# Performance work log

Measured on AMD Instinct MI355X. Metric: run time of the kernel, lower is better.

Reference implementation:

```python
import jax, jax.numpy as jnp
import numpy as np

ALPHA = 0.2   # LeakyReLU negative slope
NEG = -1e9    # mask value for non-edges


def setup_inputs() -> dict:
    key = jax.random.key(0)
    ks = jax.random.split(key, 8)
    N, Din, F, H, Dout = 4096, 512, 64, 8, 16
    adj = (jax.random.uniform(ks[0], (N, N)) < 0.01).astype(jnp.float32)
    adjacency = jnp.maximum(adj, jnp.eye(N, dtype=jnp.float32))
    X = jax.random.normal(ks[1], (N, Din), jnp.float32)
    s = lambda k, shape, fan: jax.random.normal(k, shape, jnp.float32) / np.float32(np.sqrt(fan))
    W = s(ks[2], (H, Din, F), Din)        # per-head projection, stacked
    a1 = s(ks[3], (H, F), F)              # attention vector, source half
    a2 = s(ks[4], (H, F), F)              # attention vector, target half
    Wo = s(ks[5], (H * F, Dout), H * F)   # output-layer projection
    ao1 = s(ks[6], (Dout,), Dout)
    ao2 = s(ks[7], (Dout,), Dout)
    return dict(adjacency=adjacency, X=X, W=W, a1=a1, a2=a2, Wo=Wo, ao1=ao1, ao2=ao2)


def reference(adjacency, X, W, a1, a2, Wo, ao1, ao2):
    # dropout is identity (eval mode / p=0)
    mask = adjacency > 0
    N = X.shape[0]
    # --- multi-head attention layers (concat=True -> ELU) ---
    Wh = jnp.einsum('nd,hdf->hnf', X, W)                      # [H, N, F]
    f1 = jnp.einsum('hnf,hf->hn', Wh, a1)                     # [H, N]
    f2 = jnp.einsum('hnf,hf->hn', Wh, a2)                     # [H, N]
    e = jax.nn.leaky_relu(f1[:, :, None] + f2[:, None, :], ALPHA)  # [H, N, N]
    att = jax.nn.softmax(jnp.where(mask[None], e, NEG), axis=-1)
    heads = jax.nn.elu(jnp.einsum('hnm,hmf->hnf', att, Wh))   # [H, N, F]
    cat = jnp.transpose(heads, (1, 0, 2)).reshape(N, -1)      # [N, H*F]
    # --- output attention layer (concat=False -> no ELU) ---
    Who = cat @ Wo                                            # [N, Dout]
    eo = jax.nn.leaky_relu((Who @ ao1)[:, None] + (Who @ ao2)[None, :], ALPHA)
    atto = jax.nn.softmax(jnp.where(mask, eo, NEG), axis=-1)  # [N, N]
    return atto @ Who                                         # [N, Dout]
```

## Files before the change

kernel.cpp:

```cpp
#include <hip/hip_runtime.h>
#include <hip/hip_bf16.h>

#define N_NODES 4096
#define DIN     512
#define FDIM    64
#define NHEADS  8
#define DOUT    16
#define MAXN    512

typedef __attribute__((ext_vector_type(8))) short bf16x8;
typedef __attribute__((ext_vector_type(4))) float f32x4;

static __device__ __forceinline__ float us2f(unsigned short u) {
    union { unsigned int i; float f; } cv; cv.i = ((unsigned int)u) << 16; return cv.f;
}
static __device__ __forceinline__ unsigned short f2us(float v) {
    __hip_bfloat16 b = __float2bfloat16(v);
    return *(const unsigned short*)&b;
}

__global__ __launch_bounds__(256) void setup_kernel(
    const void* __restrict__ adjv,
    const void* __restrict__ a1, const void* __restrict__ a2, const void* __restrict__ Wo,
    const void* __restrict__ ao1, const void* __restrict__ ao2,
    int* __restrict__ flag, float* __restrict__ dst,
    unsigned short* __restrict__ WtH, unsigned short* __restrict__ WtL)
{
    __shared__ int sflag;
    if (threadIdx.x == 0) {
        int f = (((const unsigned short*)adjv)[0] == 0) ? 1 : 0;
        *flag = f;
        sflag = f;
    }
    __syncthreads();
    const int f32 = sflag;
    const void* srcs[5] = { a1, a2, Wo, ao1, ao2 };
    const int   szs[5]  = { 512, 512, 8192, 16, 16 };
    int base = 0;
    for (int s = 0; s < 5; ++s) {
        if (f32) {
            for (int i = threadIdx.x; i < szs[s]; i += 256)
                dst[base + i] = ((const float*)srcs[s])[i];
        } else {
            for (int i = threadIdx.x; i < szs[s]; i += 256)
                dst[base + i] = us2f(((const unsigned short*)srcs[s])[i]);
        }
        base += szs[s];
    }
    __syncthreads();
    const float* Woc = dst + 1024;
    for (int l = threadIdx.x; l < DIN * DOUT; l += 256) {
        int d = l >> 4, j = l & 15;
        float v = Woc[l];
        unsigned short hi = f2us(v);
        WtH[j * DIN + d] = hi;
        WtL[j * DIN + d] = f2us(v - us2f(hi));
    }
}

__global__ __launch_bounds__(256) void build_nbr_kernel(
    const void* __restrict__ adj, const int* __restrict__ flag,
    int* __restrict__ cnt, int* __restrict__ nbr)
{
    const int n = blockIdx.x;
    const int f32 = *flag;
    __shared__ int c;
    if (threadIdx.x == 0) c = 0;
    __syncthreads();
    if (f32) {
        const uint4* row = (const uint4*)((const unsigned int*)adj + (size_t)n * N_NODES);
        for (int q = threadIdx.x; q < N_NODES / 4; q += 256) {
            uint4 v = row[q];
            int base = q * 4;
            if (v.x) { int p = atomicAdd(&c, 1); if (p < MAXN) nbr[(size_t)n * MAXN + p] = base + 0; }
            if (v.y) { int p = atomicAdd(&c, 1); if (p < MAXN) nbr[(size_t)n * MAXN + p] = base + 1; }
            if (v.z) { int p = atomicAdd(&c, 1); if (p < MAXN) nbr[(size_t)n * MAXN + p] = base + 2; }
            if (v.w) { int p = atomicAdd(&c, 1); if (p < MAXN) nbr[(size_t)n * MAXN + p] = base + 3; }
        }
    } else {
        const ushort4* row = (const ushort4*)((const unsigned short*)adj + (size_t)n * N_NODES);
        for (int q = threadIdx.x; q < N_NODES / 4; q += 256) {
            ushort4 v = row[q];
            int base = q * 4;
            if (v.x) { int p = atomicAdd(&c, 1); if (p < MAXN) nbr[(size_t)n * MAXN + p] = base + 0; }
            if (v.y) { int p = atomicAdd(&c, 1); if (p < MAXN) nbr[(size_t)n * MAXN + p] = base + 1; }
            if (v.z) { int p = atomicAdd(&c, 1); if (p < MAXN) nbr[(size_t)n * MAXN + p] = base + 2; }
            if (v.w) { int p = atomicAdd(&c, 1); if (p < MAXN) nbr[(size_t)n * MAXN + p] = base + 3; }
        }
    }
    __syncthreads();
    if (threadIdx.x == 0) cnt[n] = (c < MAXN) ? c : MAXN;
}

__global__ __launch_bounds__(256) void wh_mfma_kernel(
    const void* __restrict__ X, const void* __restrict__ W,
    const int* __restrict__ flag, unsigned short* __restrict__ Whb)
{
    __shared__ unsigned short Ah[64][72];
    __shared__ unsigned short Al[64][72];
    __shared__ unsigned short Bt[64][72];
    const int f32 = *flag;
    const int h  = blockIdx.x;
    const int bm = blockIdx.y;
    const int tid  = threadIdx.x;
    const int w    = tid >> 6;
    const int lane = tid & 63;
    const int quad = lane >> 4;
    const int l16  = lane & 15;
    const int r  = tid >> 2;
    const int c4 = (tid & 3) * 16;

    f32x4 acc[4];
#pragma unroll
    for (int j = 0; j < 4; ++j) acc[j] = (f32x4){0.f, 0.f, 0.f, 0.f};

    for (int k0 = 0; k0 < DIN; k0 += 64) {
        if (f32) {
            const float* xp = (const float*)X + (size_t)(bm * 64 + r) * DIN + k0 + c4;
            const float* wp = (const float*)W + (size_t)h * DIN * FDIM + (size_t)(k0 + r) * FDIM + c4;
#pragma unroll
            for (int i4 = 0; i4 < 4; ++i4) {
                float4 v4 = ((const float4*)xp)[i4];
                float vv[4] = { v4.x, v4.y, v4.z, v4.w };
#pragma unroll
                for (int t = 0; t < 4; ++t) {
                    int i = i4 * 4 + t;
                    unsigned short hi = f2us(vv[t]);
                    Ah[r][c4 + i] = hi;
                    Al[r][c4 + i] = f2us(vv[t] - us2f(hi));
                }
            }
#pragma unroll
            for (int i4 = 0; i4 < 4; ++i4) {
                float4 v4 = ((const float4*)wp)[i4];
                Bt[c4 + i4 * 4 + 0][r] = f2us(v4.x);
                Bt[c4 + i4 * 4 + 1][r] = f2us(v4.y);
                Bt[c4 + i4 * 4 + 2][r] = f2us(v4.z);
                Bt[c4 + i4 * 4 + 3][r] = f2us(v4.w);
            }
        } else {
            const unsigned short* xp = (const unsigned short*)X + (size_t)(bm * 64 + r) * DIN + k0 + c4;
            const unsigned short* wp = (const unsigned short*)W + (size_t)h * DIN * FDIM + (size_t)(k0 + r) * FDIM + c4;
#pragma unroll
            for (int i = 0; i < 16; ++i) { Ah[r][c4 + i] = xp[i]; Al[r][c4 + i] = 0; }
#pragma unroll
            for (int i = 0; i < 16; ++i) Bt[c4 + i][r] = wp[i];
        }
        __syncthreads();
#pragma unroll
        for (int kk = 0; kk < 64; kk += 32) {
            bf16x8 a_hi = *(const bf16x8*)&Ah[w * 16 + l16][kk + quad * 8];
            bf16x8 a_lo = *(const bf16x8*)&Al[w * 16 + l16][kk + quad * 8];
#pragma unroll
            for (int j = 0; j < 4; ++j) {
                bf16x8 b = *(const bf16x8*)&Bt[j * 16 + l16][kk + quad * 8];
                acc[j] = __builtin_amdgcn_mfma_f32_16x16x32_bf16(a_hi, b, acc[j], 0, 0, 0);
                acc[j] = __builtin_amdgcn_mfma_f32_16x16x32_bf16(a_lo, b, acc[j], 0, 0, 0);
            }
        }
        __syncthreads();
    }
#pragma unroll
    for (int j = 0; j < 4; ++j) {
        int col = j * 16 + l16;
#pragma unroll
        for (int rr = 0; rr < 4; ++rr) {
            int row = bm * 64 + w * 16 + quad * 4 + rr;
            Whb[((size_t)h * N_NODES + row) * FDIM + col] = f2us(acc[j][rr]);
        }
    }
}

__global__ __launch_bounds__(128) void f12_kernel(
    const unsigned short* __restrict__ Whb,
    const float* __restrict__ a1c, const float* __restrict__ a2c,
    float* __restrict__ f1, float* __restrict__ f2)
{
    int idx = blockIdx.x * 128 + threadIdx.x;
    int h = idx >> 12;
    const bf16x8* row = (const bf16x8*)(Whb + (size_t)idx * FDIM);
    float s1 = 0.f, s2 = 0.f;
#pragma unroll
    for (int q = 0; q < 8; ++q) {
        bf16x8 v8 = row[q];
#pragma unroll
        for (int t = 0; t < 8; ++t) {
            float v = us2f((unsigned short)v8[t]);
            int f = q * 8 + t;
            s1 += v * a1c[h * FDIM + f];
            s2 += v * a2c[h * FDIM + f];
        }
    }
    f1[idx] = s1;
    f2[idx] = s2;
}

__global__ __launch_bounds__(256) void attn1_kernel(
    const unsigned short* __restrict__ Whb,
    const float* __restrict__ f1, const float* __restrict__ f2,
    const int* __restrict__ cnt, const int* __restrict__ nbr,
    unsigned short* __restrict__ catb)
{
    const int n = blockIdx.x;
    const int tid = threadIdx.x;
    const int wid = tid >> 6;
    const int lane = tid & 63;
    __shared__ int sh_m[MAXN];
    __shared__ float sh_s[4][MAXN];
    const int c0 = cnt[n];
    const int c = (c0 < MAXN) ? c0 : MAXN;
    for (int k = tid; k < c; k += 256) sh_m[k] = nbr[(size_t)n * MAXN + k];
    __syncthreads();
    for (int hh = 0; hh < 2; ++hh) {
        const int h = wid * 2 + hh;
        const float f1v = f1[h * N_NODES + n];
        float mx = -1e30f;
        for (int k = lane; k < c; k += 64) {
            float s = f1v + f2[h * N_NODES + sh_m[k]];
            s = (s >= 0.f) ? s : 0.2f * s;
            sh_s[wid][k] = s;
            mx = fmaxf(mx, s);
        }
#pragma unroll
        for (int off = 32; off; off >>= 1) mx = fmaxf(mx, __shfl_xor(mx, off));
        float sum = 0.f;
        for (int k = lane; k < c; k += 64) {
            float e = __expf(sh_s[wid][k] - mx);
            sh_s[wid][k] = e;
            sum += e;
        }
#pragma unroll
        for (int off = 32; off; off >>= 1) sum += __shfl_xor(sum, off);
        const float inv = (sum > 0.f) ? 1.f / sum : 0.f;
        float acc = 0.f;
        for (int k = 0; k < c; ++k)
            acc += sh_s[wid][k] * us2f(Whb[((size_t)h * N_NODES + sh_m[k]) * FDIM + lane]);
        acc *= inv;
        acc = (acc > 0.f) ? acc : expm1f(acc);
        catb[(size_t)n * (NHEADS * FDIM) + h * FDIM + lane] = f2us(acc);
        __syncthreads();
    }
}

__global__ __launch_bounds__(64) void who_mfma_g_kernel(
    const unsigned short* __restrict__ catb,
    const unsigned short* __restrict__ WtH, const unsigned short* __restrict__ WtL,
    const float* __restrict__ ao1c, const float* __restrict__ ao2c,
    float* __restrict__ Who, float* __restrict__ g1, float* __restrict__ g2)
{
    const int lane = threadIdx.x;
    const int quad = lane >> 4, l16 = lane & 15;
    const int row0 = blockIdx.x * 16;
    f32x4 acc = (f32x4){0.f, 0.f, 0.f, 0.f};
    for (int k0 = 0; k0 < DIN; k0 += 32) {
        bf16x8 a  = *(const bf16x8*)&catb[(size_t)(row0 + l16) * DIN + k0 + quad * 8];
        bf16x8 bh = *(const bf16x8*)&WtH[l16 * DIN + k0 + quad * 8];
        bf16x8 bl = *(const bf16x8*)&WtL[l16 * DIN + k0 + quad * 8];
        acc = __builtin_amdgcn_mfma_f32_16x16x32_bf16(a, bh, acc, 0, 0, 0);
        acc = __builtin_amdgcn_mfma_f32_16x16x32_bf16(a, bl, acc, 0, 0, 0);
    }
#pragma unroll
    for (int rr = 0; rr < 4; ++rr) {
        int row = row0 + quad * 4 + rr;
        float v = acc[rr];
        Who[row * DOUT + l16] = v;
        float p1 = v * ao1c[l16];
        float p2 = v * ao2c[l16];
#pragma unroll
        for (int off = 8; off; off >>= 1) {
            p1 += __shfl_xor(p1, off);
            p2 += __shfl_xor(p2, off);
        }
        if (l16 == 0) { g1[row] = p1; g2[row] = p2; }
    }
}

__global__ __launch_bounds__(64) void attn2_kernel(
    const float* __restrict__ Who,
    const float* __restrict__ g1, const float* __restrict__ g2,
    const int* __restrict__ cnt, const int* __restrict__ nbr,
    const int* __restrict__ flag, void* __restrict__ out)
{
    const int n = blockIdx.x;
    const int lane = threadIdx.x;
    const int quad = lane >> 4, l16 = lane & 15;
    __shared__ float sh_s[MAXN];
    __shared__ int sh_m[MAXN];
    const int c0 = cnt[n];
    const int c = (c0 < MAXN) ? c0 : MAXN;
    for (int k = lane; k < c; k += 64) sh_m[k] = nbr[(size_t)n * MAXN + k];
    __syncthreads();
    const float gn = g1[n];
    float mx = -1e30f;
    for (int k = lane; k < c; k += 64) {
        float s = gn + g2[sh_m[k]];
        s = (s >= 0.f) ? s : 0.2f * s;
        sh_s[k] = s;
        mx = fmaxf(mx, s);
    }
#pragma unroll
    for (int off = 32; off; off >>= 1) mx = fmaxf(mx, __shfl_xor(mx, off));
    __syncthreads();
    float sum = 0.f;
    for (int k = lane; k < c; k += 64) {
        float e = __expf(sh_s[k] - mx);
        sh_s[k] = e;
        sum += e;
    }
#pragma unroll
    for (int off = 32; off; off >>= 1) sum += __shfl_xor(sum, off);
    __syncthreads();
    const float inv = (sum > 0.f) ? 1.f / sum : 0.f;
    float accv = 0.f;
    for (int k = quad; k < c; k += 4)
        accv += sh_s[k] * Who[sh_m[k] * DOUT + l16];
    accv += __shfl_xor(accv, 16);
    accv += __shfl_xor(accv, 32);
    if (quad == 0) {
        float v = accv * inv;
        if (*flag) ((float*)out)[n * DOUT + l16] = v;
        else       ((unsigned short*)out)[n * DOUT + l16] = f2us(v);
    }
}

__global__ void wsfail_kernel(float* __restrict__ out)
{
    if (threadIdx.x == 0) out[0] = 129.f;
}

extern "C" void kernel_launch(void* const* d_in, const int* in_sizes, int n_in,
                              void* d_out, int out_size, void* d_ws, size_t ws_size,
                              hipStream_t stream)
{
    const void* adj = d_in[0];
    const void* X   = d_in[1];
    const void* W   = d_in[2];
    const void* a1  = d_in[3];
    const void* a2  = d_in[4];
    const void* Wo  = d_in[5];
    const void* ao1 = d_in[6];
    const void* ao2 = d_in[7];

    const size_t NEEDED = 17500000;
    if (ws_size < NEEDED) { wsfail_kernel<<<1, 64, 0, stream>>>((float*)d_out); return; }

    int* flag = (int*)d_ws;
    int* cnt  = flag + 1;
    int* nbr  = cnt + 4096;
    float* smalls = (float*)(nbr + 2097152);
    float* a1c  = smalls;
    float* a2c  = smalls + 512;
    float* ao1c = smalls + 9216;
    float* ao2c = smalls + 9232;
    float* f1   = smalls + 9248;
    float* f2   = f1 + 32768;
    float* Who  = f2 + 32768;
    float* g1   = Who + 65536;
    float* g2   = g1 + 4096;
    unsigned short* Whb  = (unsigned short*)(g2 + 4096);
    unsigned short* catb = Whb + 2097152;
    unsigned short* WtH  = catb + 2097152;
    unsigned short* WtL  = WtH + 8192;

    setup_kernel<<<1, 256, 0, stream>>>(adj, a1, a2, Wo, ao1, ao2, flag, smalls, WtH, WtL);
    build_nbr_kernel<<<N_NODES, 256, 0, stream>>>(adj, flag, cnt, nbr);
    wh_mfma_kernel<<<dim3(NHEADS, N_NODES / 64), 256, 0, stream>>>(X, W, flag, Whb);
    f12_kernel<<<256, 128, 0, stream>>>(Whb, a1c, a2c, f1, f2);
    attn1_kernel<<<N_NODES, 256, 0, stream>>>(Whb, f1, f2, cnt, nbr, catb);
    who_mfma_g_kernel<<<N_NODES / 16, 64, 0, stream>>>(catb, WtH, WtL, ao1c, ao2c, Who, g1, g2);
    attn2_kernel<<<N_NODES, 64, 0, stream>>>(Who, g1, g2, cnt, nbr, flag, d_out);
}
```

Measured before the change: 183.7 us.

## Pre-split inputs in a wide prep kernel, node-major Wh, all-heads attn1

Replaces the single-block setup kernel with a grid-wide prep kernel that converts X into bf16 hi/lo halves and writes W transposed, so the Wh MFMA kernel reads operands directly from global memory without LDS staging or barriers. Wh is stored node-major ([N, H, F]), so attn1 processes all eight heads per block and each neighbor gather becomes one contiguous 1 KB row read instead of eight strided ones. The flag buffer is dropped in favor of detecting dtype from the adjacency in every kernel. This adds about 9 MB of workspace traffic for the pre-split X and skips LDS reuse of A/B tiles in the GEMM.

```diff
diff --git a/kernel.cpp b/kernel.cpp
--- a/kernel.cpp
+++ b/kernel.cpp
@@ -18,52 +18,56 @@
     __hip_bfloat16 b = __float2bfloat16(v);
     return *(const unsigned short*)&b;
 }
-
-__global__ __launch_bounds__(256) void setup_kernel(
-    const void* __restrict__ adjv,
+static __device__ __forceinline__ int is_f32(const void* adj) {
+    return (((const unsigned short*)adj)[0] == 0) ? 1 : 0;
+}
+
+__global__ __launch_bounds__(256) void prep_kernel(
+    const void* __restrict__ adj, const void* __restrict__ X, const void* __restrict__ W,
     const void* __restrict__ a1, const void* __restrict__ a2, const void* __restrict__ Wo,
     const void* __restrict__ ao1, const void* __restrict__ ao2,
-    int* __restrict__ flag, float* __restrict__ dst,
-    unsigned short* __restrict__ WtH, unsigned short* __restrict__ WtL)
-{
-    __shared__ int sflag;
-    if (threadIdx.x == 0) {
-        int f = (((const unsigned short*)adjv)[0] == 0) ? 1 : 0;
-        *flag = f;
-        sflag = f;
-    }
-    __syncthreads();
-    const int f32 = sflag;
-    const void* srcs[5] = { a1, a2, Wo, ao1, ao2 };
-    const int   szs[5]  = { 512, 512, 8192, 16, 16 };
-    int base = 0;
-    for (int s = 0; s < 5; ++s) {
-        if (f32) {
-            for (int i = threadIdx.x; i < szs[s]; i += 256)
-                dst[base + i] = ((const float*)srcs[s])[i];
-        } else {
-            for (int i = threadIdx.x; i < szs[s]; i += 256)
-                dst[base + i] = us2f(((const unsigned short*)srcs[s])[i]);
-        }
-        base += szs[s];
-    }
-    __syncthreads();
-    const float* Woc = dst + 1024;
-    for (int l = threadIdx.x; l < DIN * DOUT; l += 256) {
-        int d = l >> 4, j = l & 15;
-        float v = Woc[l];
+    unsigned short* __restrict__ Xhi, unsigned short* __restrict__ Xlo,
+    unsigned short* __restrict__ Wt,
+    unsigned short* __restrict__ WtH, unsigned short* __restrict__ WtL,
+    float* __restrict__ a1c, float* __restrict__ a2c,
+    float* __restrict__ ao1c, float* __restrict__ ao2c)
+{
+    const int f32 = is_f32(adj);
+    const int i0 = blockIdx.x * 256 + threadIdx.x;
+    const int T = gridDim.x * 256;
+    for (int i = i0; i < N_NODES * DIN; i += T) {
+        float v = f32 ? ((const float*)X)[i] : us2f(((const unsigned short*)X)[i]);
+        unsigned short hi = f2us(v);
+        Xhi[i] = hi;
+        Xlo[i] = f2us(v - us2f(hi));
+    }
+    for (int i = i0; i < NHEADS * DIN * FDIM; i += T) {
+        int hh = i >> 15, rem = i & 32767, d = rem >> 6, f = rem & 63;
+        float v = f32 ? ((const float*)W)[i] : us2f(((const unsigned short*)W)[i]);
+        Wt[((size_t)(hh * FDIM + f)) * DIN + d] = f2us(v);
+    }
+    for (int i = i0; i < DIN * DOUT; i += T) {
+        int d = i >> 4, j = i & 15;
+        float v = f32 ? ((const float*)Wo)[i] : us2f(((const unsigned short*)Wo)[i]);
         unsigned short hi = f2us(v);
         WtH[j * DIN + d] = hi;
         WtL[j * DIN + d] = f2us(v - us2f(hi));
     }
+    if (i0 < 512) {
+        a1c[i0] = f32 ? ((const float*)a1)[i0] : us2f(((const unsigned short*)a1)[i0]);
+        a2c[i0] = f32 ? ((const float*)a2)[i0] : us2f(((const unsigned short*)a2)[i0]);
+    }
+    if (i0 < 16) {
+        ao1c[i0] = f32 ? ((const float*)ao1)[i0] : us2f(((const unsigned short*)ao1)[i0]);
+        ao2c[i0] = f32 ? ((const float*)ao2)[i0] : us2f(((const unsigned short*)ao2)[i0]);
+    }
 }
 
 __global__ __launch_bounds__(256) void build_nbr_kernel(
-    const void* __restrict__ adj, const int* __restrict__ flag,
-    int* __restrict__ cnt, int* __restrict__ nbr)
+    const void* __restrict__ adj, int* __restrict__ cnt, int* __restrict__ nbr)
 {
     const int n = blockIdx.x;
-    const int f32 = *flag;
+    const int f32 = is_f32(adj);
     __shared__ int c;
     if (threadIdx.x == 0) c = 0;
     __syncthreads();
@@ -93,72 +97,34 @@
 }
 
 __global__ __launch_bounds__(256) void wh_mfma_kernel(
-    const void* __restrict__ X, const void* __restrict__ W,
-    const int* __restrict__ flag, unsigned short* __restrict__ Whb)
-{
-    __shared__ unsigned short Ah[64][72];
-    __shared__ unsigned short Al[64][72];
-    __shared__ unsigned short Bt[64][72];
-    const int f32 = *flag;
+    const unsigned short* __restrict__ Xhi, const unsigned short* __restrict__ Xlo,
+    const unsigned short* __restrict__ Wt, unsigned short* __restrict__ Whb)
+{
     const int h  = blockIdx.x;
     const int bm = blockIdx.y;
-    const int tid  = threadIdx.x;
-    const int w    = tid >> 6;
-    const int lane = tid & 63;
+    const int w    = threadIdx.x >> 6;
+    const int lane = threadIdx.x & 63;
     const int quad = lane >> 4;
     const int l16  = lane & 15;
-    const int r  = tid >> 2;
-    const int c4 = (tid & 3) * 16;
+    const int rowA = bm * 64 + w * 16 + l16;
 
     f32x4 acc[4];
 #pragma unroll
     for (int j = 0; j < 4; ++j) acc[j] = (f32x4){0.f, 0.f, 0.f, 0.f};
 
-    for (int k0 = 0; k0 < DIN; k0 += 64) {
-        if (f32) {
-            const float* xp = (const float*)X + (size_t)(bm * 64 + r) * DIN + k0 + c4;
-            const float* wp = (const float*)W + (size_t)h * DIN * FDIM + (size_t)(k0 + r) * FDIM + c4;
-#pragma unroll
-            for (int i4 = 0; i4 < 4; ++i4) {
-                float4 v4 = ((const float4*)xp)[i4];
-                float vv[4] = { v4.x, v4.y, v4.z, v4.w };
-#pragma unroll
-                for (int t = 0; t < 4; ++t) {
-                    int i = i4 * 4 + t;
-                    unsigned short hi = f2us(vv[t]);
-                    Ah[r][c4 + i] = hi;
-                    Al[r][c4 + i] = f2us(vv[t] - us2f(hi));
-                }
-            }
-#pragma unroll
-            for (int i4 = 0; i4 < 4; ++i4) {
-                float4 v4 = ((const float4*)wp)[i4];
-                Bt[c4 + i4 * 4 + 0][r] = f2us(v4.x);
-                Bt[c4 + i4 * 4 + 1][r] = f2us(v4.y);
-                Bt[c4 + i4 * 4 + 2][r] = f2us(v4.z);
-                Bt[c4 + i4 * 4 + 3][r] = f2us(v4.w);
-            }
-        } else {
-            const unsigned short* xp = (const unsigned short*)X + (size_t)(bm * 64 + r) * DIN + k0 + c4;
-            const unsigned short* wp = (const unsigned short*)W + (size_t)h * DIN * FDIM + (size_t)(k0 + r) * FDIM + c4;
-#pragma unroll
-            for (int i = 0; i < 16; ++i) { Ah[r][c4 + i] = xp[i]; Al[r][c4 + i] = 0; }
-#pragma unroll
-            for (int i = 0; i < 16; ++i) Bt[c4 + i][r] = wp[i];
-        }
-        __syncthreads();
-#pragma unroll
-        for (int kk = 0; kk < 64; kk += 32) {
-            bf16x8 a_hi = *(const bf16x8*)&Ah[w * 16 + l16][kk + quad * 8];
-            bf16x8 a_lo = *(const bf16x8*)&Al[w * 16 + l16][kk + quad * 8];
-#pragma unroll
-            for (int j = 0; j < 4; ++j) {
-                bf16x8 b = *(const bf16x8*)&Bt[j * 16 + l16][kk + quad * 8];
-                acc[j] = __builtin_amdgcn_mfma_f32_16x16x32_bf16(a_hi, b, acc[j], 0, 0, 0);
-                acc[j] = __builtin_amdgcn_mfma_f32_16x16x32_bf16(a_lo, b, acc[j], 0, 0, 0);
-            }
-        }
-        __syncthreads();
+    const unsigned short* xh = Xhi + (size_t)rowA * DIN + quad * 8;
+    const unsigned short* xl = Xlo + (size_t)rowA * DIN + quad * 8;
+    const unsigned short* wb = Wt + (size_t)h * FDIM * DIN + quad * 8;
+#pragma unroll 2
+    for (int k0 = 0; k0 < DIN; k0 += 32) {
+        bf16x8 ah = *(const bf16x8*)(xh + k0);
+        bf16x8 al = *(const bf16x8*)(xl + k0);
+#pragma unroll
+        for (int j = 0; j < 4; ++j) {
+            bf16x8 b = *(const bf16x8*)(wb + (size_t)(j * 16 + l16) * DIN + k0);
+            acc[j] = __builtin_amdgcn_mfma_f32_16x16x32_bf16(ah, b, acc[j], 0, 0, 0);
+            acc[j] = __builtin_amdgcn_mfma_f32_16x16x32_bf16(al, b, acc[j], 0, 0, 0);
+        }
     }
 #pragma unroll
     for (int j = 0; j < 4; ++j) {
@@ -166,18 +132,25 @@
 #pragma unroll
         for (int rr = 0; rr < 4; ++rr) {
             int row = bm * 64 + w * 16 + quad * 4 + rr;
-            Whb[((size_t)h * N_NODES + row) * FDIM + col] = f2us(acc[j][rr]);
-        }
-    }
-}
-
-__global__ __launch_bounds__(128) void f12_kernel(
+            Whb[((size_t)row * NHEADS + h) * FDIM + col] = f2us(acc[j][rr]);
+        }
+    }
+}
+
+__global__ __launch_bounds__(256) void f12_kernel(
     const unsigned short* __restrict__ Whb,
     const float* __restrict__ a1c, const float* __restrict__ a2c,
     float* __restrict__ f1, float* __restrict__ f2)
 {
-    int idx = blockIdx.x * 128 + threadIdx.x;
-    int h = idx >> 12;
+    __shared__ float sA1[512], sA2[512];
+    for (int i = threadIdx.x; i < 512; i += 256) {
+        int hh = i & 7, ff = i >> 3;
+        sA1[i] = a1c[hh * FDIM + ff];
+        sA2[i] = a2c[hh * FDIM + ff];
+    }
+    __syncthreads();
+    int idx = blockIdx.x * 256 + threadIdx.x;
+    int h = idx & 7, n = idx >> 3;
     const bf16x8* row = (const bf16x8*)(Whb + (size_t)idx * FDIM);
     float s1 = 0.f, s2 = 0.f;
 #pragma unroll
@@ -187,12 +160,12 @@
         for (int t = 0; t < 8; ++t) {
             float v = us2f((unsigned short)v8[t]);
             int f = q * 8 + t;
-            s1 += v * a1c[h * FDIM + f];
-            s2 += v * a2c[h * FDIM + f];
-        }
-    }
-    f1[idx] = s1;
-    f2[idx] = s2;
+            s1 += v * sA1[f * 8 + h];
+            s2 += v * sA2[f * 8 + h];
+        }
+    }
+    f1[h * N_NODES + n] = s1;
+    f2[h * N_NODES + n] = s2;
 }
 
 __global__ __launch_bounds__(256) void attn1_kernel(
@@ -203,43 +176,51 @@
 {
     const int n = blockIdx.x;
     const int tid = threadIdx.x;
-    const int wid = tid >> 6;
-    const int lane = tid & 63;
     __shared__ int sh_m[MAXN];
-    __shared__ float sh_s[4][MAXN];
+    __shared__ float sh_s[NHEADS][MAXN];
+    __shared__ float sh_inv[NHEADS];
     const int c0 = cnt[n];
     const int c = (c0 < MAXN) ? c0 : MAXN;
     for (int k = tid; k < c; k += 256) sh_m[k] = nbr[(size_t)n * MAXN + k];
     __syncthreads();
-    for (int hh = 0; hh < 2; ++hh) {
-        const int h = wid * 2 + hh;
-        const float f1v = f1[h * N_NODES + n];
-        float mx = -1e30f;
-        for (int k = lane; k < c; k += 64) {
-            float s = f1v + f2[h * N_NODES + sh_m[k]];
-            s = (s >= 0.f) ? s : 0.2f * s;
-            sh_s[wid][k] = s;
-            mx = fmaxf(mx, s);
-        }
-#pragma unroll
-        for (int off = 32; off; off >>= 1) mx = fmaxf(mx, __shfl_xor(mx, off));
-        float sum = 0.f;
-        for (int k = lane; k < c; k += 64) {
-            float e = __expf(sh_s[wid][k] - mx);
-            sh_s[wid][k] = e;
-            sum += e;
-        }
-#pragma unroll
-        for (int off = 32; off; off >>= 1) sum += __shfl_xor(sum, off);
-        const float inv = (sum > 0.f) ? 1.f / sum : 0.f;
-        float acc = 0.f;
-        for (int k = 0; k < c; ++k)
-            acc += sh_s[wid][k] * us2f(Whb[((size_t)h * N_NODES + sh_m[k]) * FDIM + lane]);
-        acc *= inv;
-        acc = (acc > 0.f) ? acc : expm1f(acc);
-        catb[(size_t)n * (NHEADS * FDIM) + h * FDIM + lane] = f2us(acc);
-        __syncthreads();
-    }
+    const int h = tid >> 5;
+    const int l32 = tid & 31;
+    const float f1v = f1[h * N_NODES + n];
+    float mx = -1e30f;
+    for (int k = l32; k < c; k += 32) {
+        float s = f1v + f2[h * N_NODES + sh_m[k]];
+        s = (s >= 0.f) ? s : 0.2f * s;
+        sh_s[h][k] = s;
+        mx = fmaxf(mx, s);
+    }
+#pragma unroll
+    for (int off = 16; off; off >>= 1) mx = fmaxf(mx, __shfl_xor(mx, off));
+    __syncthreads();
+    float sum = 0.f;
+    for (int k = l32; k < c; k += 32) {
+        float e = __expf(sh_s[h][k] - mx);
+        sh_s[h][k] = e;
+        sum += e;
+    }
+#pragma unroll
+    for (int off = 16; off; off >>= 1) sum += __shfl_xor(sum, off);
+    if (l32 == 0) sh_inv[h] = (sum > 0.f) ? 1.f / sum : 0.f;
+    __syncthreads();
+    float a0 = 0.f, a1v = 0.f;
+    const unsigned int* base = (const unsigned int*)Whb;
+#pragma unroll 4
+    for (int k = 0; k < c; ++k) {
+        unsigned int u = base[(size_t)sh_m[k] * 256 + tid];
+        float wgt = sh_s[h][k];
+        a0  += wgt * us2f((unsigned short)(u & 0xFFFFu));
+        a1v += wgt * us2f((unsigned short)(u >> 16));
+    }
+    const float inv = sh_inv[h];
+    a0 *= inv; a1v *= inv;
+    a0  = (a0  > 0.f) ? a0  : expm1f(a0);
+    a1v = (a1v > 0.f) ? a1v : expm1f(a1v);
+    unsigned int o = (unsigned int)f2us(a0) | ((unsigned int)f2us(a1v) << 16);
+    ((unsigned int*)catb)[(size_t)n * 256 + tid] = o;
 }
 
 __global__ __launch_bounds__(64) void who_mfma_g_kernel(
@@ -276,10 +257,11 @@
 }
 
 __global__ __launch_bounds__(64) void attn2_kernel(
+    const void* __restrict__ adj,
     const float* __restrict__ Who,
     const float* __restrict__ g1, const float* __restrict__ g2,
     const int* __restrict__ cnt, const int* __restrict__ nbr,
-    const int* __restrict__ flag, void* __restrict__ out)
+    void* __restrict__ out)
 {
     const int n = blockIdx.x;
     const int lane = threadIdx.x;
@@ -318,8 +300,8 @@
     accv += __shfl_xor(accv, 32);
     if (quad == 0) {
         float v = accv * inv;
-        if (*flag) ((float*)out)[n * DOUT + l16] = v;
-        else       ((unsigned short*)out)[n * DOUT + l16] = f2us(v);
+        if (is_f32(adj)) ((float*)out)[n * DOUT + l16] = v;
+        else             ((unsigned short*)out)[n * DOUT + l16] = f2us(v);
     }
 }
 
@@ -341,32 +323,34 @@
     const void* ao1 = d_in[6];
     const void* ao2 = d_in[7];
 
-    const size_t NEEDED = 17500000;
+    const size_t NEEDED = 26400000;
     if (ws_size < NEEDED) { wsfail_kernel<<<1, 64, 0, stream>>>((float*)d_out); return; }
 
-    int* flag = (int*)d_ws;
-    int* cnt  = flag + 1;
-    int* nbr  = cnt + 4096;
-    float* smalls = (float*)(nbr + 2097152);
-    float* a1c  = smalls;
-    float* a2c  = smalls + 512;
-    float* ao1c = smalls + 9216;
-    float* ao2c = smalls + 9232;
-    float* f1   = smalls + 9248;
+    int*   cnt  = (int*)d_ws;
+    int*   nbr  = cnt + 4096;
+    float* a1c  = (float*)(nbr + 2097152);
+    float* a2c  = a1c + 512;
+    float* ao1c = a2c + 512;
+    float* ao2c = ao1c + 16;
+    float* f1   = ao2c + 16;
     float* f2   = f1 + 32768;
     float* Who  = f2 + 32768;
     float* g1   = Who + 65536;
     float* g2   = g1 + 4096;
     unsigned short* Whb  = (unsigned short*)(g2 + 4096);
     unsigned short* catb = Whb + 2097152;
-    unsigned short* WtH  = catb + 2097152;
+    unsigned short* Xhi  = catb + 2097152;
+    unsigned short* Xlo  = Xhi + 2097152;
+    unsigned short* Wt   = Xlo + 2097152;
+    unsigned short* WtH  = Wt + 262144;
     unsigned short* WtL  = WtH + 8192;
 
-    setup_kernel<<<1, 256, 0, stream>>>(adj, a1, a2, Wo, ao1, ao2, flag, smalls, WtH, WtL);
-    build_nbr_kernel<<<N_NODES, 256, 0, stream>>>(adj, flag, cnt, nbr);
-    wh_mfma_kernel<<<dim3(NHEADS, N_NODES / 64), 256, 0, stream>>>(X, W, flag, Whb);
-    f12_kernel<<<256, 128, 0, stream>>>(Whb, a1c, a2c, f1, f2);
+    prep_kernel<<<1024, 256, 0, stream>>>(adj, X, W, a1, a2, Wo, ao1, ao2,
+                                          Xhi, Xlo, Wt, WtH, WtL, a1c, a2c, ao1c, ao2c);
+    build_nbr_kernel<<<N_NODES, 256, 0, stream>>>(adj, cnt, nbr);
+    wh_mfma_kernel<<<dim3(NHEADS, N_NODES / 64), 256, 0, stream>>>(Xhi, Xlo, Wt, Whb);
+    f12_kernel<<<128, 256, 0, stream>>>(Whb, a1c, a2c, f1, f2);
     attn1_kernel<<<N_NODES, 256, 0, stream>>>(Whb, f1, f2, cnt, nbr, catb);
     who_mfma_g_kernel<<<N_NODES / 16, 64, 0, stream>>>(catb, WtH, WtL, ao1c, ao2c, Who, g1, g2);
-    attn2_kernel<<<N_NODES, 64, 0, stream>>>(Who, g1, g2, cnt, nbr, flag, d_out);
-}
+    attn2_kernel<<<N_NODES, 64, 0, stream>>>(adj, Who, g1, g2, cnt, nbr, d_out);
+}
```

Result: faster. 177.4 us (-3.4%).
